# Kernel optimization log

Measured on AMD Instinct MI355X. Metric: run time of the kernel, lower is better.

The kernel has to match this reference:

```python
import jax, jax.numpy as jnp
import numpy as np

H = 128          # GRU hidden size (fixed in module)
EPS = 1e-8       # torch CosineSimilarity eps


def _gru_dir(x, w_ih, w_hh, b_ih, b_hh, reverse):
    # x: [B, L, D]; torch GRU gate math, single direction
    B = x.shape[0]
    gx = jnp.einsum('bld,gd->blg', x, w_ih) + b_ih  # [B, L, 3H]

    def step(h, gx_t):
        gh = h @ w_hh.T + b_hh
        xr, xz, xn = jnp.split(gx_t, 3, axis=-1)
        hr, hz, hn = jnp.split(gh, 3, axis=-1)
        r = jax.nn.sigmoid(xr + hr)
        z = jax.nn.sigmoid(xz + hz)
        n = jnp.tanh(xn + r * hn)
        h_new = (1.0 - z) * n + z * h
        return h_new, h_new

    h0 = jnp.zeros((B, H), x.dtype)
    h_last, outs = jax.lax.scan(step, h0, jnp.swapaxes(gx, 0, 1), reverse=reverse)
    return jnp.swapaxes(outs, 0, 1), h_last  # [B, L, H], [B, H]


def _bigru(x, p):
    # p = (w_ih_f, w_hh_f, b_ih_f, b_hh_f, w_ih_b, w_hh_b, b_ih_b, b_hh_b)
    of, hf = _gru_dir(x, p[0], p[1], p[2], p[3], False)
    ob, hb = _gru_dir(x, p[4], p[5], p[6], p[7], True)
    # outs concat = torch bidirectional output; [hf, hb] concat == h_n.transpose(1,0).reshape(B,-1)
    return jnp.concatenate([of, ob], axis=-1), jnp.concatenate([hf, hb], axis=-1)


def _cosnorm(x):
    return x / jnp.maximum(jnp.linalg.norm(x, axis=-1, keepdims=True), EPS)


def _forward(context, options, rnn_p, attn_p):
    ctx_outs, ctx_h = _bigru(context, rnn_p)  # [B, L1, 2H], [B, 2H]

    def per_option(option):  # option: [B, L2, D]
        opt_outs, _ = _bigru(option, rnn_p)  # [B, L2, 2H]
        # cosine-similarity attention == matmul of L2-normalized vectors
        # (replaces the original O(B*L2*L1*2H) repeated tensors, same math)
        att = jnp.einsum('bqh,bkh->bqk', _cosnorm(opt_outs), _cosnorm(ctx_outs))  # [B, L2, L1]
        att = jax.nn.softmax(att, axis=2)  # softmax over context positions (dim=2)
        att_opt = jnp.einsum('bqk,bkh->bqh', att, ctx_outs)  # bmm -> [B, L2, 2H]
        cat = jnp.concatenate([att_opt, opt_outs], axis=-1)  # [B, L2, 4H]
        _, ao_h = _bigru(cat, attn_p)  # [B, 2H]
        num = jnp.sum(ctx_h * ao_h, axis=-1)
        den = jnp.maximum(jnp.linalg.norm(ctx_h, axis=-1), EPS) * \
              jnp.maximum(jnp.linalg.norm(ao_h, axis=-1), EPS)
        return num / den  # [B]

    logits = jax.vmap(per_option)(jnp.swapaxes(options, 0, 1))  # [N, B]
    return jax.nn.softmax(logits.T, axis=1)  # [B, N]


def setup_inputs():
    key = jax.random.key(0)
    ks = jax.random.split(key, 24)
    B, L1, L2, N, D = 64, 512, 50, 10, 300
    inp = {
        'context': jax.random.normal(ks[0], (B, L1, D), jnp.float32),
        'context_lens': jax.random.randint(ks[1], (B,), 1, L1),
        'options': jax.random.normal(ks[2], (B, N, L2, D), jnp.float32),
        'option_lens': jax.random.randint(ks[3], (B, N), 1, L2),
    }
    names = ['rw_ih_f', 'rw_hh_f', 'rb_ih_f', 'rb_hh_f',
             'rw_ih_b', 'rw_hh_b', 'rb_ih_b', 'rb_hh_b',
             'aw_ih_f', 'aw_hh_f', 'ab_ih_f', 'ab_hh_f',
             'aw_ih_b', 'aw_hh_b', 'ab_ih_b', 'ab_hh_b']
    shapes = [(3 * H, D), (3 * H, H), (3 * H,), (3 * H,)] * 2 + \
             [(3 * H, 4 * H), (3 * H, H), (3 * H,), (3 * H,)] * 2
    for i, (n, sh) in enumerate(zip(names, shapes)):
        inp[n] = jax.random.normal(ks[4 + i], sh, jnp.float32) * 0.05
    return inp


def reference(context, context_lens, options, option_lens,
              rw_ih_f, rw_hh_f, rb_ih_f, rb_hh_f,
              rw_ih_b, rw_hh_b, rb_ih_b, rb_hh_b,
              aw_ih_f, aw_hh_f, ab_ih_f, ab_hh_f,
              aw_ih_b, aw_hh_b, ab_ih_b, ab_hh_b):
    rnn_p = (rw_ih_f, rw_hh_f, rb_ih_f, rb_hh_f, rw_ih_b, rw_hh_b, rb_ih_b, rb_hh_b)
    attn_p = (aw_ih_f, aw_hh_f, ab_ih_f, ab_hh_f, aw_ih_b, aw_hh_b, ab_ih_b, ab_hh_b)
    return _forward(context, options, rnn_p, attn_p)
```

## Files before the change

kernel.cpp:

```cpp
#include <hip/hip_runtime.h>
#include <math.h>

#define EPS 1e-8f

typedef _Float16 h2_t __attribute__((ext_vector_type(2)));
typedef _Float16 half8 __attribute__((ext_vector_type(8)));
typedef float f32x4 __attribute__((ext_vector_type(4)));

__device__ __forceinline__ float fsig(float x)  { return 1.0f / (1.0f + __expf(-x)); }
__device__ __forceinline__ float ftanh(float x) { return 1.0f - 2.0f / (1.0f + __expf(2.0f * x)); }

__device__ __forceinline__ float qsum4(float x) {
    int y1 = __builtin_amdgcn_update_dpp(
        0, __builtin_bit_cast(int, x), 0xB1, 0xF, 0xF, true);
    float s1 = x + __builtin_bit_cast(float, y1);
    int y2 = __builtin_amdgcn_update_dpp(
        0, __builtin_bit_cast(int, s1), 0x4E, 0xF, 0xF, true);
    return s1 + __builtin_bit_cast(float, y2);
}

__global__ __launch_bounds__(256) void prep_w_k(
    const float* __restrict__ rwf, const float* __restrict__ rwb,
    const float* __restrict__ awf, const float* __restrict__ awb,
    const float* __restrict__ rbf, const float* __restrict__ rbb,
    const float* __restrict__ abf, const float* __restrict__ abb,
    const float* __restrict__ rhf, const float* __restrict__ rhb,
    const float* __restrict__ ahf, const float* __restrict__ ahb,
    _Float16* __restrict__ wrh, _Float16* __restrict__ wah,
    _Float16* __restrict__ wr16, _Float16* __restrict__ wa16,
    float* __restrict__ br, float* __restrict__ ba)
{
    int idx = blockIdx.x * 256 + threadIdx.x;
    if (idx < 768 * 320) {
        int g = idx / 320, k = idx % 320;
        float v = 0.f;
        if (k < 300) v = (g < 384) ? rwf[g * 300 + k] : rwb[(g - 384) * 300 + k];
        wrh[idx] = (_Float16)v;
    }
    if (idx < 768 * 512) {
        int g = idx / 512, k = idx % 512;
        wah[idx] = (_Float16)((g < 384) ? awf[g * 512 + k] : awb[(g - 384) * 512 + k]);
    }
    if (idx < 2 * 384 * 128) {
        int d = idx / 49152, r = idx % 49152;
        wr16[idx] = (_Float16)(d ? rhb[r] : rhf[r]);
        wa16[idx] = (_Float16)(d ? ahb[r] : ahf[r]);
    }
    if (idx < 768) {
        br[idx] = (idx < 384) ? rbf[idx] : rbb[idx - 384];
        ba[idx] = (idx < 384) ? abf[idx] : abb[idx - 384];
    }
}

__global__ __launch_bounds__(256) void conv_k(
    const float* __restrict__ ctx, const float* __restrict__ opt,
    _Float16* __restrict__ ctxh, _Float16* __restrict__ opth)
{
    int idx = blockIdx.x * 256 + threadIdx.x;
    if (idx < 32768 * 320) {
        int r = idx / 320, k = idx % 320;
        ctxh[idx] = (k < 300) ? (_Float16)ctx[r * 300 + k] : (_Float16)0.f;
    }
    if (idx < 32000 * 320) {
        int r = idx / 320, k = idx % 320;
        opth[idx] = (k < 300) ? (_Float16)opt[r * 300 + k] : (_Float16)0.f;
    }
}

template <bool TRBS, bool SPLITA, bool HASBIAS>
__global__ __launch_bounds__(256, 4) void hgemm_k(
    const _Float16* __restrict__ A, const _Float16* __restrict__ A2,
    const _Float16* __restrict__ B, const float* __restrict__ bias,
    _Float16* __restrict__ C, int M, int N, int K,
    int lda, int ldb, int ldc, long sA, long sB, int bdiv, long sC)
{
    const int jn = blockIdx.x * 64;
    const int im = blockIdx.y * 64;
    const int z  = blockIdx.z;
    const _Float16* Bb = B + (size_t)(z / bdiv) * sB;
    _Float16* Cb = C + (size_t)z * sC;

    __shared__ __align__(16) _Float16 As[64 * 64];
    __shared__ __align__(16) _Float16 Bs[64 * 64];

    const int tid  = threadIdx.x;
    const int arow = tid >> 2;
    const int akof = (tid & 3) * 8;
    const int lane = tid & 63;
    const int wv   = tid >> 6;
    const int wm   = (wv & 1) * 32;
    const int wn   = (wv >> 1) * 32;
    const int fm   = lane & 15;
    const int quad = lane >> 4;

    f32x4 acc[2][2];
#pragma unroll
    for (int a = 0; a < 2; a++)
#pragma unroll
        for (int b = 0; b < 2; b++) acc[a][b] = (f32x4)0.f;

    for (int k0 = 0; k0 < K; k0 += 64) {
        {
            const int row = im + arow;
#pragma unroll
            for (int hh = 0; hh < 2; hh++) {
                half8 av = (half8)(_Float16)0.f;
                const int kg = k0 + akof + 32 * hh;
                if (row < M) {
                    if constexpr (SPLITA) {
                        const _Float16* Ah  = A + (size_t)z * sA;
                        const _Float16* A2h = A2 + (size_t)z * sA;
                        const _Float16* ap = (kg < 256)
                            ? (Ah + (size_t)row * lda + kg)
                            : (A2h + (size_t)row * lda + (kg - 256));
                        av = *(const half8*)ap;
                    } else {
                        av = *(const half8*)(A + (size_t)z * sA + (size_t)row * lda + kg);
                    }
                }
                *(half8*)&As[arow * 64 + akof + 32 * hh] = av;
            }
        }
        if constexpr (!TRBS) {
#pragma unroll
            for (int hh = 0; hh < 2; hh++) {
                half8 bv = *(const half8*)(Bb + (size_t)(jn + arow) * ldb
                                           + k0 + akof + 32 * hh);
                *(half8*)&Bs[arow * 64 + akof + 32 * hh] = bv;
            }
        } else {
            const int kk = tid >> 3, noff = (tid & 7) * 8;
            half8 bv0 = *(const half8*)(Bb + (size_t)(k0 + kk) * ldb + jn + noff);
            half8 bv1 = *(const half8*)(Bb + (size_t)(k0 + kk + 32) * ldb + jn + noff);
#pragma unroll
            for (int e = 0; e < 8; e++) {
                Bs[(noff + e) * 64 + kk]      = bv0[e];
                Bs[(noff + e) * 64 + kk + 32] = bv1[e];
            }
        }
        __syncthreads();

        const _Float16* Asp = As + (wm + fm) * 64 + quad * 8;
        const _Float16* Bsp = Bs + (wn + fm) * 64 + quad * 8;
#pragma unroll
        for (int kh = 0; kh < 64; kh += 32) {
            half8 a0 = *(const half8*)(Asp + kh);
            half8 a1 = *(const half8*)(Asp + 16 * 64 + kh);
            half8 b0 = *(const half8*)(Bsp + kh);
            half8 b1 = *(const half8*)(Bsp + 16 * 64 + kh);
            acc[0][0] = __builtin_amdgcn_mfma_f32_16x16x32_f16(a0, b0, acc[0][0], 0, 0, 0);
            acc[0][1] = __builtin_amdgcn_mfma_f32_16x16x32_f16(a0, b1, acc[0][1], 0, 0, 0);
            acc[1][0] = __builtin_amdgcn_mfma_f32_16x16x32_f16(a1, b0, acc[1][0], 0, 0, 0);
            acc[1][1] = __builtin_amdgcn_mfma_f32_16x16x32_f16(a1, b1, acc[1][1], 0, 0, 0);
        }
        __syncthreads();
    }

#pragma unroll
    for (int tm = 0; tm < 2; tm++) {
#pragma unroll
        for (int tn = 0; tn < 2; tn++) {
            const int col  = jn + wn + tn * 16 + fm;
            const int row0 = im + wm + tm * 16 + quad * 4;
            const float bv = HASBIAS ? bias[col] : 0.f;
#pragma unroll
            for (int r = 0; r < 4; r++) {
                const int row = row0 + r;
                if (row < M)
                    Cb[(size_t)row * ldc + col] = (_Float16)(acc[tm][tn][r] + bv);
            }
        }
    }
}

__global__ __launch_bounds__(256, 2) void gru_rec_k(
    const _Float16* __restrict__ gx,
    const _Float16* __restrict__ whh16,
    const float* __restrict__ bhh_f, const float* __restrict__ bhh_b,
    _Float16* __restrict__ outs_h, float* __restrict__ hfin, int L)
{
    const int dir = blockIdx.x & 1;
    const int s   = blockIdx.x >> 1;
    const int t   = threadIdx.x;
    const int w   = t >> 6;
    const int l   = t & 63;
    const int i0  = w * 16 + (l >> 2);
    const int i1  = i0 + 64;
    const int kq  = l & 3;
    const _Float16* Wd = whh16 + (size_t)dir * 49152;
    const float* bh = dir ? bhh_b : bhh_f;

    h2_t w2[2][3][16];
#pragma unroll
    for (int oo = 0; oo < 2; oo++)
#pragma unroll
        for (int j = 0; j < 3; j++) {
            const _Float16* Wr = Wd + (size_t)(i0 + 64 * oo + 128 * j) * 128 + 32 * kq;
#pragma unroll
            for (int q = 0; q < 16; q++)
                w2[oo][j][q] = *(const h2_t*)(Wr + 2 * q);
        }
    const float b00 = bh[i0], b01 = bh[i0 + 128], b02 = bh[i0 + 256];
    const float b10 = bh[i1], b11 = bh[i1 + 128], b12 = bh[i1 + 256];

    __shared__ __align__(16) _Float16 h1[2][128];
    __shared__ __align__(16) _Float16 gxs[32][384];
    __shared__ __align__(16) _Float16 outb[32][128];
    if (t < 128) h1[0][t] = (_Float16)0.f;
    float hprev0 = 0.f, hprev1 = 0.f;

    for (int t0 = 0; t0 < L; t0 += 32) {
        const int Tc = (L - t0 < 32) ? (L - t0) : 32;
#pragma unroll
        for (int r = 0; r < 6; r++) {
            const int q = t + 256 * r;
            if (q < Tc * 48) {
                const int j = q / 48, off = (q % 48) * 8;
                const int tt = dir ? (L - 1 - (t0 + j)) : (t0 + j);
                *(half8*)&gxs[j][off] =
                    *(const half8*)(gx + ((size_t)s * L + tt) * 768 + dir * 384 + off);
            }
        }
        __syncthreads();

        for (int j = 0; j < Tc; j++) {
            const int cb = (t0 + j) & 1;
            const h2_t* hp = (const h2_t*)&h1[cb][32 * kq];
            float a00 = 0.f, a01 = 0.f, a02 = 0.f;
            float a10 = 0.f, a11 = 0.f, a12 = 0.f;
#pragma unroll
            for (int q = 0; q < 16; q++) {
                h2_t hq = hp[q];
                a00 = __builtin_amdgcn_fdot2(w2[0][0][q], hq, a00, false);
                a01 = __builtin_amdgcn_fdot2(w2[0][1][q], hq, a01, false);
                a02 = __builtin_amdgcn_fdot2(w2[0][2][q], hq, a02, false);
                a10 = __builtin_amdgcn_fdot2(w2[1][0][q], hq, a10, false);
                a11 = __builtin_amdgcn_fdot2(w2[1][1][q], hq, a11, false);
                a12 = __builtin_amdgcn_fdot2(w2[1][2][q], hq, a12, false);
            }
            a00 = qsum4(a00); a01 = qsum4(a01); a02 = qsum4(a02);
            a10 = qsum4(a10); a11 = qsum4(a11); a12 = qsum4(a12);
            const float xc00 = (float)gxs[j][i0];
            const float xc01 = (float)gxs[j][i0 + 128];
            const float xc02 = (float)gxs[j][i0 + 256];
            const float xc10 = (float)gxs[j][i1];
            const float xc11 = (float)gxs[j][i1 + 128];
            const float xc12 = (float)gxs[j][i1 + 256];
            const float r0  = fsig(xc00 + a00 + b00);
            const float z0  = fsig(xc01 + a01 + b01);
            const float n0  = ftanh(xc02 + r0 * (a02 + b02));
            const float hn0 = (1.0f - z0) * n0 + z0 * hprev0;
            const float r1  = fsig(xc10 + a10 + b10);
            const float z1  = fsig(xc11 + a11 + b11);
            const float n1  = ftanh(xc12 + r1 * (a12 + b12));
            const float hn1 = (1.0f - z1) * n1 + z1 * hprev1;
            hprev0 = hn0;
            hprev1 = hn1;
            if (kq == 0) {
                h1[cb ^ 1][i0] = (_Float16)hn0;
                h1[cb ^ 1][i1] = (_Float16)hn1;
                outb[j][i0]    = (_Float16)hn0;
                outb[j][i1]    = (_Float16)hn1;
            }
            __syncthreads();
        }

        if (outs_h) {
#pragma unroll
            for (int r = 0; r < 2; r++) {
                const int q = t + 256 * r;
                if (q < Tc * 16) {
                    const int j = q / 16, off = (q % 16) * 8;
                    const int tt = dir ? (L - 1 - (t0 + j)) : (t0 + j);
                    *(half8*)(outs_h + ((size_t)s * L + tt) * 256 + dir * 128 + off) =
                        *(const half8*)&outb[j][off];
                }
            }
        }
    }
    if (hfin && kq == 0) {
        hfin[(size_t)s * 256 + dir * 128 + i0] = hprev0;
        hfin[(size_t)s * 256 + dir * 128 + i1] = hprev1;
    }
}

__global__ __launch_bounds__(256) void rowinv_k(const _Float16* __restrict__ x,
                                                float* __restrict__ rinv)
{
    const int row = blockIdx.x;
    float v = (float)x[(size_t)row * 256 + threadIdx.x];
    float ss = v * v;
#pragma unroll
    for (int o = 32; o > 0; o >>= 1) ss += __shfl_down(ss, o);
    __shared__ float ps[4];
    if ((threadIdx.x & 63) == 0) ps[threadIdx.x >> 6] = ss;
    __syncthreads();
    if (threadIdx.x == 0)
        rinv[row] = 1.0f / fmaxf(sqrtf(ps[0] + ps[1] + ps[2] + ps[3]), EPS);
}

__global__ __launch_bounds__(256) void att_softmax_k(
    _Float16* __restrict__ att, const float* __restrict__ rinv_opt_l,
    const float* __restrict__ rinv_ctx, int sbase)
{
    const int row = blockIdx.x;
    const int b = (sbase + row / 50) / 10;
    _Float16* p = att + (size_t)row * 512;
    const float* rc = rinv_ctx + b * 512;
    const float sA = rinv_opt_l[row];
    const int t = threadIdx.x;

    float v0 = (float)p[t]       * (sA * rc[t]);
    float v1 = (float)p[t + 256] * (sA * rc[t + 256]);

    __shared__ float red[4];
    float m = fmaxf(v0, v1);
#pragma unroll
    for (int o = 32; o > 0; o >>= 1) m = fmaxf(m, __shfl_down(m, o));
    if ((t & 63) == 0) red[t >> 6] = m;
    __syncthreads();
    m = fmaxf(fmaxf(red[0], red[1]), fmaxf(red[2], red[3]));
    float e0 = __expf(v0 - m), e1 = __expf(v1 - m);
    float ssum = e0 + e1;
#pragma unroll
    for (int o = 32; o > 0; o >>= 1) ssum += __shfl_down(ssum, o);
    __syncthreads();
    if ((t & 63) == 0) red[t >> 6] = ssum;
    __syncthreads();
    float inv = 1.0f / (red[0] + red[1] + red[2] + red[3]);
    p[t]       = (_Float16)(e0 * inv);
    p[t + 256] = (_Float16)(e1 * inv);
}

__global__ __launch_bounds__(256) void logits_k(const float* __restrict__ ch,
                                                const float* __restrict__ ah,
                                                float* __restrict__ logits)
{
    const int s = blockIdx.x;
    const int b = s / 10;
    const int t = threadIdx.x;
    float a = ch[b * 256 + t];
    float c = ah[(size_t)s * 256 + t];
    float num = a * c, na = a * a, nc = c * c;
#pragma unroll
    for (int o = 32; o > 0; o >>= 1) {
        num += __shfl_down(num, o);
        na  += __shfl_down(na,  o);
        nc  += __shfl_down(nc,  o);
    }
    __shared__ float pn[4], pa[4], pc[4];
    if ((t & 63) == 0) { pn[t >> 6] = num; pa[t >> 6] = na; pc[t >> 6] = nc; }
    __syncthreads();
    if (t == 0) {
        float sn = pn[0] + pn[1] + pn[2] + pn[3];
        float sa = pa[0] + pa[1] + pa[2] + pa[3];
        float sc = pc[0] + pc[1] + pc[2] + pc[3];
        logits[s] = sn / (fmaxf(sqrtf(sa), EPS) * fmaxf(sqrtf(sc), EPS));
    }
}

__global__ __launch_bounds__(64) void soft10_k(const float* __restrict__ logits,
                                               float* __restrict__ out)
{
    const int b = blockIdx.x;
    const int t = threadIdx.x;
    __shared__ float v[10];
    if (t < 10) v[t] = logits[b * 10 + t];
    __syncthreads();
    if (t < 10) {
        float m = v[0];
#pragma unroll
        for (int i = 1; i < 10; i++) m = fmaxf(m, v[i]);
        float ssum = 0.f;
#pragma unroll
        for (int i = 0; i < 10; i++) ssum += __expf(v[i] - m);
        out[b * 10 + t] = __expf(v[t] - m) / ssum;
    }
}

extern "C" void kernel_launch(void* const* d_in, const int* in_sizes, int n_in,
                              void* d_out, int out_size, void* d_ws, size_t ws_size,
                              hipStream_t stream)
{
    const float* context = (const float*)d_in[0];
    const float* options = (const float*)d_in[2];
    const float* rw_ih_f = (const float*)d_in[4];
    const float* rw_hh_f = (const float*)d_in[5];
    const float* rb_ih_f = (const float*)d_in[6];
    const float* rb_hh_f = (const float*)d_in[7];
    const float* rw_ih_b = (const float*)d_in[8];
    const float* rw_hh_b = (const float*)d_in[9];
    const float* rb_ih_b = (const float*)d_in[10];
    const float* rb_hh_b = (const float*)d_in[11];
    const float* aw_ih_f = (const float*)d_in[12];
    const float* aw_hh_f = (const float*)d_in[13];
    const float* ab_ih_f = (const float*)d_in[14];
    const float* ab_hh_f = (const float*)d_in[15];
    const float* aw_ih_b = (const float*)d_in[16];
    const float* aw_hh_b = (const float*)d_in[17];
    const float* ab_ih_b = (const float*)d_in[18];
    const float* ab_hh_b = (const float*)d_in[19];

    const size_t persist = 15222144;
    static const int cands[6][2] = {{1,2},{1,4},{2,4},{2,8},{4,16},{8,16}};
    int CC = 8, OC = 16;
    for (int idx = 0; idx < 6; idx++) {
        size_t bc_ = 64 / cands[idx][0], sc_ = 640 / cands[idx][1];
        size_t p = bc_ * 196608;
        if (sc_ * 32000 > p) p = sc_ * 32000;
        if ((persist + p + 2 * sc_ * 6400) * 4 <= ws_size) {
            CC = cands[idx][0]; OC = cands[idx][1]; break;
        }
    }
    const int bc = 64 / CC;
    const int sc = 640 / OC;
    size_t poolsz = (size_t)bc * 196608;
    if ((size_t)sc * 32000 > poolsz) poolsz = (size_t)sc * 32000;

    float* ws = (float*)d_ws;
    size_t off = 0;
    _Float16* wrh   = (_Float16*)(ws + off); off += 122880;
    float*    br    = ws + off;              off += 768;
    _Float16* wah   = (_Float16*)(ws + off); off += 196608;
    float*    ba    = ws + off;              off += 768;
    _Float16* wr16  = (_Float16*)(ws + off); off += 49152;
    _Float16* wa16  = (_Float16*)(ws + off); off += 49152;
    _Float16* couts = (_Float16*)(ws + off); off += 4194304;
    float*    ctxhf = ws + off;              off += 16384;
    float*    aohf  = ws + off;              off += 163840;
    float*    logits= ws + off;              off += 640;
    float*    rinvc = ws + off;              off += 32768;
    float*    rinvo = ws + off;              off += 32000;
    _Float16* ctxh  = (_Float16*)(ws + off); off += 5242880;
    _Float16* opth  = (_Float16*)(ws + off); off += 5120000;
    _Float16* POOL  = (_Float16*)(ws + off); off += poolsz;
    _Float16* P2H   = (_Float16*)(ws + off); off += (size_t)sc * 6400;
    _Float16* P3H   = (_Float16*)(ws + off); off += (size_t)sc * 6400;
    _Float16* ATT   = POOL + (size_t)sc * 38400;

    prep_w_k<<<1536, 256, 0, stream>>>(rw_ih_f, rw_ih_b, aw_ih_f, aw_ih_b,
                                       rb_ih_f, rb_ih_b, ab_ih_f, ab_ih_b,
                                       rw_hh_f, rw_hh_b, aw_hh_f, aw_hh_b,
                                       wrh, wah, wr16, wa16, br, ba);
    conv_k<<<40960, 256, 0, stream>>>(context, options, ctxh, opth);

    for (int c = 0; c < CC; c++) {
        const int Mc = bc * 512;
        hgemm_k<false, false, true><<<dim3(12, Mc / 64, 1), 256, 0, stream>>>(
            ctxh + (size_t)c * Mc * 320, nullptr, wrh, br, POOL,
            Mc, 768, 320, 320, 320, 768, 0, 0, 1, 0);
        gru_rec_k<<<2 * bc, 256, 0, stream>>>(
            POOL, wr16, rb_hh_f, rb_hh_b,
            couts + (size_t)c * Mc * 256, ctxhf + (size_t)c * bc * 256, 512);
    }

    rowinv_k<<<32768, 256, 0, stream>>>(couts, rinvc);

    for (int o = 0; o < OC; o++) {
        const int base = o * sc;
        const int Mo = sc * 50;
        const _Float16* ctxB = couts + (size_t)(base / 10) * 131072;

        hgemm_k<false, false, true><<<dim3(12, (Mo + 63) / 64, 1), 256, 0, stream>>>(
            opth + (size_t)base * 50 * 320, nullptr, wrh, br, POOL,
            Mo, 768, 320, 320, 320, 768, 0, 0, 1, 0);
        gru_rec_k<<<2 * sc, 256, 0, stream>>>(
            POOL, wr16, rb_hh_f, rb_hh_b, P2H, nullptr, 50);
        rowinv_k<<<Mo, 256, 0, stream>>>(P2H, rinvo + (size_t)base * 50);
        hgemm_k<false, false, false><<<dim3(8, 1, sc), 256, 0, stream>>>(
            P2H, nullptr, ctxB, nullptr, ATT,
            50, 512, 256, 256, 256, 512, 12800, 131072, 10, 25600);
        att_softmax_k<<<Mo, 256, 0, stream>>>(ATT, rinvo + (size_t)base * 50,
                                              rinvc, base);
        hgemm_k<true, false, false><<<dim3(4, 1, sc), 256, 0, stream>>>(
            ATT, nullptr, ctxB, nullptr, P3H,
            50, 256, 512, 512, 256, 256, 25600, 131072, 10, 12800);
        hgemm_k<false, true, true><<<dim3(12, (Mo + 63) / 64, 1), 256, 0, stream>>>(
            P3H, P2H, wah, ba, POOL,
            Mo, 768, 512, 256, 512, 768, 0, 0, 1, 0);
        gru_rec_k<<<2 * sc, 256, 0, stream>>>(
            POOL, wa16, ab_hh_f, ab_hh_b, nullptr, aohf + (size_t)base * 256, 50);
    }

    logits_k<<<640, 256, 0, stream>>>(ctxhf, aohf, logits);
    soft10_k<<<64, 64, 0, stream>>>(logits, (float*)d_out);
}
```

Baseline: 1.166 ms.

## Use MFMA 16x16x32 for GRU recurrent matvec instead of fdot2 with DPP reduction

Rewrites the per-step hidden-to-hidden matvec in the GRU recurrence kernel to use MFMA 16x16x32 f16 instructions. The hidden vector is broadcast as the A operand across all 16 rows, and the weights are held in registers as half8 B fragments. This replaces 96 fdot2 ops and the DPP cross-lane reductions per step, shortening the serial per-timestep latency. Only one row of each 16x16 MFMA output is used, so most of the matrix compute is wasted, and MFMA latency may dominate at this tiny size.

```diff
diff --git a/kernel.cpp b/kernel.cpp
--- a/kernel.cpp
+++ b/kernel.cpp
@@ -9,15 +9,6 @@
 
 __device__ __forceinline__ float fsig(float x)  { return 1.0f / (1.0f + __expf(-x)); }
 __device__ __forceinline__ float ftanh(float x) { return 1.0f - 2.0f / (1.0f + __expf(2.0f * x)); }
-
-__device__ __forceinline__ float qsum4(float x) {
-    int y1 = __builtin_amdgcn_update_dpp(
-        0, __builtin_bit_cast(int, x), 0xB1, 0xF, 0xF, true);
-    float s1 = x + __builtin_bit_cast(float, y1);
-    int y2 = __builtin_amdgcn_update_dpp(
-        0, __builtin_bit_cast(int, s1), 0x4E, 0xF, 0xF, true);
-    return s1 + __builtin_bit_cast(float, y2);
-}
 
 __global__ __launch_bounds__(256) void prep_w_k(
     const float* __restrict__ rwf, const float* __restrict__ rwb,
@@ -184,30 +175,33 @@
     const int t   = threadIdx.x;
     const int w   = t >> 6;
     const int l   = t & 63;
-    const int i0  = w * 16 + (l >> 2);
-    const int i1  = i0 + 64;
-    const int kq  = l & 3;
+    const int c   = l & 15;
+    const int rg  = l >> 4;
+    const int i0  = w * 32 + c;
+    const int i1  = i0 + 16;
     const _Float16* Wd = whh16 + (size_t)dir * 49152;
     const float* bh = dir ? bhh_b : bhh_f;
 
-    h2_t w2[2][3][16];
-#pragma unroll
-    for (int oo = 0; oo < 2; oo++)
-#pragma unroll
-        for (int j = 0; j < 3; j++) {
-            const _Float16* Wr = Wd + (size_t)(i0 + 64 * oo + 128 * j) * 128 + 32 * kq;
-#pragma unroll
-            for (int q = 0; q < 16; q++)
-                w2[oo][j][q] = *(const h2_t*)(Wr + 2 * q);
-        }
-    const float b00 = bh[i0], b01 = bh[i0 + 128], b02 = bh[i0 + 256];
-    const float b10 = bh[i1], b11 = bh[i1 + 128], b12 = bh[i1 + 256];
+    half8 wb[3][2][4];
+#pragma unroll
+    for (int p = 0; p < 3; p++)
+#pragma unroll
+        for (int u = 0; u < 2; u++) {
+            const int gate = p * 128 + w * 32 + u * 16 + c;
+#pragma unroll
+            for (int kf = 0; kf < 4; kf++)
+                wb[p][u][kf] =
+                    *(const half8*)(Wd + (size_t)gate * 128 + kf * 32 + rg * 8);
+        }
+    const float br0 = bh[i0],       br1 = bh[i1];
+    const float bz0 = bh[i0 + 128], bz1 = bh[i1 + 128];
+    const float bn0 = bh[i0 + 256], bn1 = bh[i1 + 256];
 
     __shared__ __align__(16) _Float16 h1[2][128];
     __shared__ __align__(16) _Float16 gxs[32][384];
     __shared__ __align__(16) _Float16 outb[32][128];
     if (t < 128) h1[0][t] = (_Float16)0.f;
-    float hprev0 = 0.f, hprev1 = 0.f;
+    float hp0 = 0.f, hp1 = 0.f;
 
     for (int t0 = 0; t0 < L; t0 += 32) {
         const int Tc = (L - t0 < 32) ? (L - t0) : 32;
@@ -225,38 +219,38 @@
 
         for (int j = 0; j < Tc; j++) {
             const int cb = (t0 + j) & 1;
-            const h2_t* hp = (const h2_t*)&h1[cb][32 * kq];
-            float a00 = 0.f, a01 = 0.f, a02 = 0.f;
-            float a10 = 0.f, a11 = 0.f, a12 = 0.f;
-#pragma unroll
-            for (int q = 0; q < 16; q++) {
-                h2_t hq = hp[q];
-                a00 = __builtin_amdgcn_fdot2(w2[0][0][q], hq, a00, false);
-                a01 = __builtin_amdgcn_fdot2(w2[0][1][q], hq, a01, false);
-                a02 = __builtin_amdgcn_fdot2(w2[0][2][q], hq, a02, false);
-                a10 = __builtin_amdgcn_fdot2(w2[1][0][q], hq, a10, false);
-                a11 = __builtin_amdgcn_fdot2(w2[1][1][q], hq, a11, false);
-                a12 = __builtin_amdgcn_fdot2(w2[1][2][q], hq, a12, false);
-            }
-            a00 = qsum4(a00); a01 = qsum4(a01); a02 = qsum4(a02);
-            a10 = qsum4(a10); a11 = qsum4(a11); a12 = qsum4(a12);
-            const float xc00 = (float)gxs[j][i0];
-            const float xc01 = (float)gxs[j][i0 + 128];
-            const float xc02 = (float)gxs[j][i0 + 256];
-            const float xc10 = (float)gxs[j][i1];
-            const float xc11 = (float)gxs[j][i1 + 128];
-            const float xc12 = (float)gxs[j][i1 + 256];
-            const float r0  = fsig(xc00 + a00 + b00);
-            const float z0  = fsig(xc01 + a01 + b01);
-            const float n0  = ftanh(xc02 + r0 * (a02 + b02));
-            const float hn0 = (1.0f - z0) * n0 + z0 * hprev0;
-            const float r1  = fsig(xc10 + a10 + b10);
-            const float z1  = fsig(xc11 + a11 + b11);
-            const float n1  = ftanh(xc12 + r1 * (a12 + b12));
-            const float hn1 = (1.0f - z1) * n1 + z1 * hprev1;
-            hprev0 = hn0;
-            hprev1 = hn1;
-            if (kq == 0) {
+            half8 af[4];
+#pragma unroll
+            for (int kf = 0; kf < 4; kf++)
+                af[kf] = *(const half8*)&h1[cb][kf * 32 + rg * 8];
+            f32x4 acc[3][2];
+#pragma unroll
+            for (int p = 0; p < 3; p++)
+#pragma unroll
+                for (int u = 0; u < 2; u++) {
+                    f32x4 a = (f32x4)0.f;
+#pragma unroll
+                    for (int kf = 0; kf < 4; kf++)
+                        a = __builtin_amdgcn_mfma_f32_16x16x32_f16(
+                                af[kf], wb[p][u][kf], a, 0, 0, 0);
+                    acc[p][u] = a;
+                }
+            const float xr0 = (float)gxs[j][i0];
+            const float xr1 = (float)gxs[j][i1];
+            const float xz0 = (float)gxs[j][i0 + 128];
+            const float xz1 = (float)gxs[j][i1 + 128];
+            const float xn0 = (float)gxs[j][i0 + 256];
+            const float xn1 = (float)gxs[j][i1 + 256];
+            const float r0 = fsig(xr0 + acc[0][0][0] + br0);
+            const float r1 = fsig(xr1 + acc[0][1][0] + br1);
+            const float z0 = fsig(xz0 + acc[1][0][0] + bz0);
+            const float z1 = fsig(xz1 + acc[1][1][0] + bz1);
+            const float q0 = ftanh(xn0 + r0 * (acc[2][0][0] + bn0));
+            const float q1 = ftanh(xn1 + r1 * (acc[2][1][0] + bn1));
+            const float hn0 = (1.0f - z0) * q0 + z0 * hp0;
+            const float hn1 = (1.0f - z1) * q1 + z1 * hp1;
+            hp0 = hn0; hp1 = hn1;
+            if (rg == 0) {
                 h1[cb ^ 1][i0] = (_Float16)hn0;
                 h1[cb ^ 1][i1] = (_Float16)hn1;
                 outb[j][i0]    = (_Float16)hn0;
@@ -278,9 +272,10 @@
             }
         }
     }
-    if (hfin && kq == 0) {
-        hfin[(size_t)s * 256 + dir * 128 + i0] = hprev0;
-        hfin[(size_t)s * 256 + dir * 128 + i1] = hprev1;
+    if (hfin && rg == 0) {
+        float* hf = hfin + (size_t)s * 256 + dir * 128;
+        hf[i0] = hp0;
+        hf[i1] = hp1;
     }
 }
 
```

Measured after the change: 1.133 ms. 1.03x faster.
